# Kernel tuning notes

Measured on AMD Instinct MI355X. Metric: run time of the kernel, lower is better.

Reference implementation:

```python
import jax, jax.numpy as jnp
import numpy as np
import math

ENC_MAX = 64
DEC_MAX = 128


def _tran_mask(M):
    # faithful reconstruction of self.tran and self.mask buffers
    fs = math.log(DEC_MAX / (DEC_MAX + ENC_MAX))  # fixed_shift_p
    fe = math.log(ENC_MAX / (DEC_MAX + ENC_MAX))  # fixed_emit_p
    i = np.arange(M)[:, None]
    j = np.arange(M)[None, :]
    tran = np.where(i + j < M, (M - (i + j) - 1) * fs + fe, 0.0).astype(np.float32)
    # mask_br: -inf where i+j >= M (anti-diagonal i+j==M-1 stays 0)
    mask = np.where(i + j >= M, -np.inf, 0.0).astype(np.float32)
    return jnp.asarray(tran), jnp.asarray(mask)


def _lstm(xs, Wih, Whh, bih, bhh):
    # xs: [L, in]; torch LSTM gate order i,f,g,o; batch=1 handled as unbatched
    H = Whh.shape[1]
    def step(carry, xt):
        h, c = carry
        g = Wih @ xt + bih + Whh @ h + bhh  # [4H]
        i, f, gg, o = jnp.split(g, 4)
        c = jax.nn.sigmoid(f) * c + jax.nn.sigmoid(i) * jnp.tanh(gg)
        h = jax.nn.sigmoid(o) * jnp.tanh(c)
        return (h, c), h
    _, hs = jax.lax.scan(step, (jnp.zeros((H,), xs.dtype), jnp.zeros((H,), xs.dtype)), xs)
    return hs  # [L, H]


def setup_inputs() -> dict:
    key = jax.random.key(0)
    ks = jax.random.split(key, 16)
    V, E, H, K, T = 32000, 100, 512, ENC_MAX, DEC_MAX
    def p(k, shape, scale):
        return jax.random.normal(k, shape, dtype=jnp.float32) * scale
    return {
        "x": jax.random.randint(ks[0], (1, K), 0, V),
        "y": jax.random.randint(ks[1], (1, T), 0, V),
        "emb": p(ks[2], (V, E), 0.1),
        "enc_Wih": p(ks[3], (4 * H, E), 1.0 / np.sqrt(E)),
        "enc_Whh": p(ks[4], (4 * H, H), 1.0 / np.sqrt(H)),
        "enc_bih": jnp.zeros((4 * H,), jnp.float32),
        "enc_bhh": jnp.zeros((4 * H,), jnp.float32),
        "dec_Wih": p(ks[5], (4 * H, E), 1.0 / np.sqrt(E)),
        "dec_Whh": p(ks[6], (4 * H, H), 1.0 / np.sqrt(H)),
        "dec_bih": jnp.zeros((4 * H,), jnp.float32),
        "dec_bhh": jnp.zeros((4 * H,), jnp.float32),
        "Weh": p(ks[7], (E, 2 * H), 1.0 / np.sqrt(2 * H)),  # emit_hidden
        "beh": jnp.zeros((E,), jnp.float32),
        "Wem": p(ks[8], (V, E), 1.0 / np.sqrt(E)),  # emit
        "bem": jnp.zeros((V,), jnp.float32),
    }


def reference(x, y, emb, enc_Wih, enc_Whh, enc_bih, enc_bhh,
              dec_Wih, dec_Whh, dec_bih, dec_bhh, Weh, beh, Wem, bem):
    K = x.shape[1]
    T = y.shape[1]
    x_emb = emb[x[0]]            # [K, E]
    y_emb = emb[y[0]]            # [T, E]
    Eenc = _lstm(x_emb, enc_Wih, enc_Whh, enc_bih, enc_bhh)  # [K, H]
    D = _lstm(y_emb, dec_Wih, dec_Whh, dec_bih, dec_bhh)     # [T, H]

    tran, mask = _tran_mask(ENC_MAX)
    tranm = tran[ENC_MAX - K:, :K] + mask[ENC_MAX - K:, :K]  # [K, K]

    # emissions for all steps at once (joint = cat(E, D_{t-1}) -> relu -> emit -> log_softmax -> gather word_t)
    H = Eenc.shape[1]
    We_E, We_D = Weh[:, :H], Weh[:, H:]
    hpre = jax.nn.relu(Eenc @ We_E.T + (D[:T - 1] @ We_D.T)[:, None, :] + beh)  # [T-1, K, E]
    logits = jnp.einsum('tke,ve->tkv', hpre, Wem) + bem                          # [T-1, K, V]
    words = y[0, 1:]                                                             # [T-1]
    gathered = jnp.take_along_axis(logits, words[:, None, None], axis=2)[..., 0]  # [T-1, K]
    emission = gathered - jax.scipy.special.logsumexp(logits, axis=2)             # [T-1, K]

    def step(pre_alpha, em_t):
        scores = pre_alpha[:, None] + tranm            # [K(i), K(j)]
        mx = jnp.max(scores, axis=0)                   # [K]
        ind = jnp.argmax(scores, axis=0).astype(jnp.int32)
        mx = jnp.flip(mx)                              # self.flip
        ind = jnp.flip(ind)
        new = mx + em_t
        return new, ind

    pre_alpha, inds = jax.lax.scan(step, jnp.zeros((K,), jnp.float32), emission)
    indices = jnp.concatenate([jnp.zeros((1, K), jnp.int32), inds], axis=0)  # [T, K]

    val = pre_alpha[K - 1]  # align_last

    def bstep(ind, idx_row):
        nind = idx_row[ind]
        return nind, nind
    _, alignments = jax.lax.scan(bstep, jnp.int32(K - 1), indices, reverse=True)  # [T]
    return alignments, val
```

## Files before the change

kernel.cpp:

```cpp
#include <hip/hip_runtime.h>


#define K_ENC 64
#define HID   512
#define EMB   100
#define VOC   32000
#define G4    2048

typedef __attribute__((ext_vector_type(8))) short  short8;
typedef __attribute__((ext_vector_type(4))) float  f32x4;
typedef __attribute__((ext_vector_type(4))) int    i32x4;
typedef unsigned long long u64;

#define LOG2E 1.4426950408889634f
#define LN2   0.6931471805599453f

__device__ __forceinline__ unsigned short f2bf(float f) {
  union { float f; unsigned u; } x; x.f = f;
  unsigned r = x.u + 0x7FFFu + ((x.u >> 16) & 1u);
  return (unsigned short)(r >> 16);
}

__device__ __forceinline__ float fast_sigmoid(float x) {
  return __builtin_amdgcn_rcpf(1.f + __builtin_amdgcn_exp2f(-LOG2E * x));
}
__device__ __forceinline__ float fast_tanh(float x) {
  return 1.f - 2.f * __builtin_amdgcn_rcpf(1.f + __builtin_amdgcn_exp2f(2.f * LOG2E * x));
}

#define OFF_PAD   0
#define OFF_HBUF  256
#define OFF_G0E   4352
#define OFF_G0D   135424
#define OFF_EENC  395520
#define OFF_D     428288
#define OFF_EWE   493312
#define OFF_DWD   499712
#define OFF_BEM   512412
#define OFF_SUM   544412
#define OFF_EM    552540
#define OFF_WEM   560668

#define PREP_G0_BLKS 1528
__global__ __launch_bounds__(256) void kPrep0(const int* __restrict__ x, const int* __restrict__ y,
                    const float* __restrict__ emb,
                    const float* __restrict__ eWih, const float* __restrict__ ebih,
                    const float* __restrict__ ebhh,
                    const float* __restrict__ dWih, const float* __restrict__ dbih,
                    const float* __restrict__ dbhh,
                    float* __restrict__ ws) {
  const int b = blockIdx.x;
  const int tid = threadIdx.x;
  if (b < PREP_G0_BLKS) {
    int gid = b * 256 + tid;
    const int enc_total = K_ENC * G4;
    if (gid >= enc_total + 127 * G4) return;
    bool enc = gid < enc_total;
    int loc = enc ? gid : gid - enc_total;
    int t = loc >> 11, r = loc & (G4 - 1);
    int tok = enc ? x[t] : y[t];
    const float* Wr = (enc ? eWih : dWih) + r * EMB;
    const float* er = emb + tok * EMB;
    float s = 0.f;
    #pragma unroll 4
    for (int e = 0; e < EMB; ++e) s += er[e] * Wr[e];
    s += enc ? (ebih[r] + ebhh[r]) : (dbih[r] + dbhh[r]);
    ws[(enc ? OFF_G0E : OFF_G0D) + t * G4 + r] = s;
  } else {
    int gid = (b - PREP_G0_BLKS) * 256 + tid;
    if (gid < 4352) ws[gid] = 0.f;
    else if (gid < 4352 + 127 * 64) ws[OFF_SUM + gid - 4352] = 0.f;
  }
}

#define STEP_GUARD 16384

__global__ __launch_bounds__(512, 2) void kLstm(const float* __restrict__ eWhh,
                                                const float* __restrict__ dWhh,
                                                const float* __restrict__ Wem,
                                                const float* __restrict__ bem,
                                                float* __restrict__ ws) {
  const int b = blockIdx.x;
  const int tid = threadIdx.x;
  if (b >= 64) {
    int gid = (b - 64) * 512 + tid;
    int vt = gid >> 11;
    int kb = (gid >> 9) & 3;
    int L  = (gid >> 3) & 63;
    int j  = gid & 7;
    int v = vt * 16 + (L & 15);
    int k = kb * 32 + ((L >> 4) << 3) + j;
    float val = (k < EMB) ? Wem[v * EMB + k] : 0.f;
    ((unsigned short*)(ws + OFF_WEM))[gid] = f2bf(val);
    if (gid < VOC) ws[OFF_BEM + gid] = bem[gid] * LOG2E;
    return;
  }
  const int grp = b >> 5;
  const int wg  = b & 31;
  const float* __restrict__ Whh = grp ? dWhh : eWhh;
  const float* __restrict__ G0  = ws + (grp ? OFF_G0D : OFF_G0E);
  float* hs = ws + (grp ? OFF_D : OFF_EENC);
  u64* hb = (u64*)(ws + OFF_HBUF) + grp * 1024;
  const int steps = grp ? 127 : K_ENC;
  const int jl = tid >> 5, sub = tid & 31;
  const int j = wg * 16 + jl;
  __shared__ float h_lds[32 * 20];

  float cst = 0.f;
  for (int t = 0; t < steps; ++t) {
    float4 w4[16];
    #pragma unroll
    for (int g = 0; g < 4; ++g)
      #pragma unroll
      for (int q = 0; q < 4; ++q)
        w4[g * 4 + q] = *(const float4*)&Whh[(g * HID + j) * HID + sub * 16 + q * 4];
    float g0i = G0[t * G4 + j];
    float g0f = G0[t * G4 + HID + j];
    float g0g = G0[t * G4 + 2 * HID + j];
    float g0o = G0[t * G4 + 3 * HID + j];
    if (tid < 256) {
      const u64* src = hb + (t & 1) * 512 + tid * 2;
      i32x4 v;
      int guard = 0;
      for (;;) {
        asm volatile("global_load_dwordx4 %0, %1, off sc0 sc1\n\t"
                     "s_waitcnt vmcnt(0)"
                     : "=v"(v) : "v"(src) : "memory");
        if ((v[1] == t && v[3] == t) || ++guard >= STEP_GUARD) break;
        __builtin_amdgcn_s_sleep(1);
      }
      int k0 = tid * 2, k1 = k0 + 1;
      union { int u; float f; } c0, c1; c0.u = v[0]; c1.u = v[2];
      h_lds[(k0 >> 4) * 20 + (k0 & 15)] = c0.f;
      h_lds[(k1 >> 4) * 20 + (k1 & 15)] = c1.f;
    }
    __syncthreads();
    float h[16];
    #pragma unroll
    for (int kk = 0; kk < 16; ++kk) h[kk] = h_lds[sub * 20 + kk];
    float p0 = 0.f, p1 = 0.f, p2 = 0.f, p3 = 0.f;
    #pragma unroll
    for (int q = 0; q < 4; ++q) {
      p0 += w4[0+q].x*h[q*4+0] + w4[0+q].y*h[q*4+1] + w4[0+q].z*h[q*4+2] + w4[0+q].w*h[q*4+3];
      p1 += w4[4+q].x*h[q*4+0] + w4[4+q].y*h[q*4+1] + w4[4+q].z*h[q*4+2] + w4[4+q].w*h[q*4+3];
      p2 += w4[8+q].x*h[q*4+0] + w4[8+q].y*h[q*4+1] + w4[8+q].z*h[q*4+2] + w4[8+q].w*h[q*4+3];
      p3 += w4[12+q].x*h[q*4+0] + w4[12+q].y*h[q*4+1] + w4[12+q].z*h[q*4+2] + w4[12+q].w*h[q*4+3];
    }
    #pragma unroll
    for (int d = 1; d <= 16; d <<= 1) {
      p0 += __shfl_xor(p0, d); p1 += __shfl_xor(p1, d);
      p2 += __shfl_xor(p2, d); p3 += __shfl_xor(p3, d);
    }
    float si = fast_sigmoid(g0i + p0);
    float sf = fast_sigmoid(g0f + p1);
    float gG = fast_tanh(g0g + p2);
    float so = fast_sigmoid(g0o + p3);
    cst = sf * cst + si * gG;
    float hn = so * fast_tanh(cst);
    if (sub == 0) {
      union { float f; unsigned u; } hu; hu.f = hn;
      u64 pack = ((u64)(unsigned)(t + 1) << 32) | (u64)hu.u;
      atomicExch(&hb[((t + 1) & 1) * 512 + j], pack);
      hs[t * HID + j] = hn;
    }
    __syncthreads();
  }
}

__global__ __launch_bounds__(256) void kProj(const float* __restrict__ Weh,
                                             const float* __restrict__ beh,
                                             float* __restrict__ ws) {
  int bid = blockIdx.x;
  bool enc = bid < K_ENC;
  int row = enc ? bid : bid - K_ENC;
  const float* in = ws + (enc ? OFF_EENC : OFF_D) + row * HID;
  __shared__ float sin_[HID];
  int tid = threadIdx.x;
  sin_[tid] = in[tid]; sin_[tid + 256] = in[tid + 256];
  __syncthreads();
  if (tid < EMB) {
    const float* wr = Weh + tid * 1024 + (enc ? 0 : HID);
    float s = 0.f;
    #pragma unroll 4
    for (int h = 0; h < HID; ++h) s += sin_[h] * wr[h];
    if (!enc) s += beh[tid];
    ws[(enc ? OFF_EWE : OFF_DWD) + row * EMB + tid] = s * LOG2E;
  }
}

__global__ __launch_bounds__(256) void kLogits(float* __restrict__ ws) {
  const int tg = blockIdx.x >> 3;
  const int chunk = blockIdx.x & 7;
  const int tid = threadIdx.x;
  const int lane = tid & 63;
  const int wv = tid >> 6;
  const int quad = lane >> 4, l15 = lane & 15;
  __shared__ __align__(16) unsigned short A[2][64 * 128];
  const float* EWe = ws + OFF_EWE;
  const int t0 = tg * 2;
  const int t1v = (t0 + 1 <= 126) ? (t0 + 1) : 126;
  const float* DWd0 = ws + OFF_DWD + t0 * EMB;
  const float* DWd1 = ws + OFF_DWD + t1v * EMB;
  for (int idx = tid; idx < 64 * 128; idx += 256) {
    int m = idx >> 7, k = idx & 127;
    float hv0 = 0.f, hv1 = 0.f;
    if (k < EMB) {
      float e = EWe[m * EMB + k];
      float s0 = e + DWd0[k]; hv0 = s0 > 0.f ? s0 : 0.f;
      float s1 = e + DWd1[k]; hv1 = s1 > 0.f ? s1 : 0.f;
    }
    A[0][idx] = f2bf(hv0);
    A[1][idx] = f2bf(hv1);
  }
  __syncthreads();
  short8 af[2][4][4];
  #pragma unroll
  for (int ts = 0; ts < 2; ++ts)
    #pragma unroll
    for (int mt = 0; mt < 4; ++mt)
      #pragma unroll
      for (int kb = 0; kb < 4; ++kb)
        af[ts][mt][kb] = *(const short8*)&A[ts][(mt * 16 + l15) * 128 + kb * 32 + quad * 8];
  const unsigned short* wem = (const unsigned short*)(ws + OFF_WEM);
  const float* bem_s = ws + OFF_BEM;
  float rs[2][4][4];
  #pragma unroll
  for (int ts = 0; ts < 2; ++ts)
    #pragma unroll
    for (int a = 0; a < 4; ++a)
      #pragma unroll
      for (int c = 0; c < 4; ++c) rs[ts][a][c] = 0.f;
  int vt = chunk * 250 + wv;
  short8 nb0, nb1, nb2, nb3; float nbi;
  nb0 = *(const short8*)&wem[(vt * 4 + 0) * 512 + lane * 8];
  nb1 = *(const short8*)&wem[(vt * 4 + 1) * 512 + lane * 8];
  nb2 = *(const short8*)&wem[(vt * 4 + 2) * 512 + lane * 8];
  nb3 = *(const short8*)&wem[(vt * 4 + 3) * 512 + lane * 8];
  nbi = bem_s[vt * 16 + l15];
  for (int ii = wv; ii < 250; ii += 4) {
    short8 cb0 = nb0, cb1 = nb1, cb2 = nb2, cb3 = nb3;
    float cbi = nbi;
    int nvt = vt + 4;
    if (ii + 4 < 250) {
      nb0 = *(const short8*)&wem[(nvt * 4 + 0) * 512 + lane * 8];
      nb1 = *(const short8*)&wem[(nvt * 4 + 1) * 512 + lane * 8];
      nb2 = *(const short8*)&wem[(nvt * 4 + 2) * 512 + lane * 8];
      nb3 = *(const short8*)&wem[(nvt * 4 + 3) * 512 + lane * 8];
      nbi = bem_s[nvt * 16 + l15];
    }
    #pragma unroll
    for (int ts = 0; ts < 2; ++ts) {
      f32x4 acc[4];
      #pragma unroll
      for (int mt = 0; mt < 4; ++mt) acc[mt] = (f32x4){cbi, cbi, cbi, cbi};
      #pragma unroll
      for (int mt = 0; mt < 4; ++mt) {
        acc[mt] = __builtin_amdgcn_mfma_f32_16x16x32_bf16(af[ts][mt][0], cb0, acc[mt], 0, 0, 0);
        acc[mt] = __builtin_amdgcn_mfma_f32_16x16x32_bf16(af[ts][mt][1], cb1, acc[mt], 0, 0, 0);
        acc[mt] = __builtin_amdgcn_mfma_f32_16x16x32_bf16(af[ts][mt][2], cb2, acc[mt], 0, 0, 0);
        acc[mt] = __builtin_amdgcn_mfma_f32_16x16x32_bf16(af[ts][mt][3], cb3, acc[mt], 0, 0, 0);
      }
      #pragma unroll
      for (int mt = 0; mt < 4; ++mt)
        #pragma unroll
        for (int r = 0; r < 4; ++r)
          rs[ts][mt][r] += __builtin_amdgcn_exp2f(acc[mt][r]);
    }
    vt = nvt;
  }
  #pragma unroll
  for (int d = 1; d < 16; d <<= 1)
    #pragma unroll
    for (int ts = 0; ts < 2; ++ts)
      #pragma unroll
      for (int mt = 0; mt < 4; ++mt)
        #pragma unroll
        for (int r = 0; r < 4; ++r)
          rs[ts][mt][r] += __shfl_xor(rs[ts][mt][r], d);
  if (l15 == 0) {
    #pragma unroll
    for (int ts = 0; ts < 2; ++ts) {
      int t = t0 + ts;
      if (t <= 126) {
        float* sum = ws + OFF_SUM + t * 64;
        #pragma unroll
        for (int mt = 0; mt < 4; ++mt)
          #pragma unroll
          for (int r = 0; r < 4; ++r)
            atomicAdd(&sum[mt * 16 + quad * 4 + r], rs[ts][mt][r]);
      }
    }
  }
}

__global__ __launch_bounds__(256) void kEmission(const int* __restrict__ y,
                                                 const float* __restrict__ Wem,
                                                 float* __restrict__ ws) {
  int gid = blockIdx.x * 256 + threadIdx.x;
  if (gid >= 127 * 64) return;
  int t = gid >> 6, m = gid & 63;
  const float* ew = ws + OFF_EWE + m * EMB;
  const float* dw = ws + OFF_DWD + t * EMB;
  int wt = y[t + 1];
  const float* wr = Wem + wt * EMB;
  float s = ws[OFF_BEM + wt];
  #pragma unroll 4
  for (int e = 0; e < EMB; ++e) {
    float h = ew[e] + dw[e];
    h = h > 0.f ? h : 0.f;
    s += h * wr[e];
  }
  ws[OFF_EM + gid] = LN2 * (s - __builtin_amdgcn_logf(ws[OFF_SUM + gid]));
}

__global__ __launch_bounds__(256) void kViterbi(const float* __restrict__ ws, float* __restrict__ out) {
  __shared__ float em_lds[127 * 64];
  __shared__ int   inds[128 * 64];
  __shared__ float sval;
  const int tid = threadIdx.x;
  for (int i = tid; i < 127 * 64; i += 256) em_lds[i] = ws[OFF_EM + i];
  if (tid < 64) inds[tid] = 0;
  __syncthreads();
  if (tid < 64) {
    const int j = tid;
    const float fs = -0.4054651081081644f;
    const float fe = -1.0986122886681098f;
    float pa = 0.f;
    float emnext = em_lds[j];
    for (int t = 0; t < 127; ++t) {
      float emc = emnext;
      if (t < 126) emnext = em_lds[(t + 1) * 64 + j];
      float v = fmaf(-fs, (float)j, pa);
      int idx = j;
      #pragma unroll
      for (int d = 1; d < 64; d <<= 1) {
        float vv = __shfl_up(v, d);
        int   ii = __shfl_up(idx, d);
        bool cur = v > vv;
        v   = cur ? v : vv;
        idx = cur ? idx : ii;
      }
      pa = v + fe + fs * (float)j + emc;
      inds[(t + 1) * 64 + j] = idx;
    }
    if (j == 63) sval = pa;
  }
  __syncthreads();
  if (tid == 0) {
    int ind = 63;
    for (int t = 127; t >= 0; --t) {
      ind = inds[t * 64 + ind];
      out[t] = (float)ind;
    }
    out[128] = sval;
  }
}

extern "C" void kernel_launch(void* const* d_in, const int* in_sizes, int n_in,
                              void* d_out, int out_size, void* d_ws, size_t ws_size,
                              hipStream_t stream) {
  const int*   x    = (const int*)d_in[0];
  const int*   y    = (const int*)d_in[1];
  const float* emb  = (const float*)d_in[2];
  const float* eWih = (const float*)d_in[3];
  const float* eWhh = (const float*)d_in[4];
  const float* ebih = (const float*)d_in[5];
  const float* ebhh = (const float*)d_in[6];
  const float* dWih = (const float*)d_in[7];
  const float* dWhh = (const float*)d_in[8];
  const float* dbih = (const float*)d_in[9];
  const float* dbhh = (const float*)d_in[10];
  const float* Weh  = (const float*)d_in[11];
  const float* beh  = (const float*)d_in[12];
  const float* Wem  = (const float*)d_in[13];
  const float* bem  = (const float*)d_in[14];
  float* ws  = (float*)d_ws;
  float* out = (float*)d_out;

  hipLaunchKernelGGL(kPrep0,    dim3(PREP_G0_BLKS + 49), dim3(256), 0, stream,
                     x, y, emb, eWih, ebih, ebhh, dWih, dbih, dbhh, ws);
  hipLaunchKernelGGL(kLstm,     dim3(64 + 8000), dim3(512), 0, stream, eWhh, dWhh, Wem, bem, ws);
  hipLaunchKernelGGL(kProj,     dim3(191),   dim3(256), 0, stream, Weh, beh, ws);
  hipLaunchKernelGGL(kLogits,   dim3(512),   dim3(256), 0, stream, ws);
  hipLaunchKernelGGL(kEmission, dim3(32),    dim3(256), 0, stream, y, Wem, ws);
  hipLaunchKernelGGL(kViterbi,  dim3(1),     dim3(256), 0, stream, ws, out);
}
```

Before: 507.8 us.

## Fuse emit-hidden projection into LSTM recurrence and pad logits LDS rows

Removes the separate kProj launch. The projection of each hidden state onto Weh now runs inside the persistent LSTM blocks: the upper four waves of each block compute up to four projection outputs from the h vector already staged in LDS, one step behind, with one extra loop iteration to finish the last row. This saves a kernel launch and re-reading the hidden states, at the cost of one more spin-wait step and extra register pressure in the latency-critical recurrence. Separately, kLogits pads its LDS A-tile rows to 136 elements to reduce bank conflicts on the short8 fragment loads.

```diff
diff --git a/kernel.cpp b/kernel.cpp
--- a/kernel.cpp
+++ b/kernel.cpp
@@ -79,6 +79,8 @@
                                                 const float* __restrict__ dWhh,
                                                 const float* __restrict__ Wem,
                                                 const float* __restrict__ bem,
+                                                const float* __restrict__ Weh,
+                                                const float* __restrict__ beh,
                                                 float* __restrict__ ws) {
   const int b = blockIdx.x;
   const int tid = threadIdx.x;
@@ -100,24 +102,43 @@
   const float* __restrict__ Whh = grp ? dWhh : eWhh;
   const float* __restrict__ G0  = ws + (grp ? OFF_G0D : OFF_G0E);
   float* hs = ws + (grp ? OFF_D : OFF_EENC);
+  float* proj = ws + (grp ? OFF_DWD : OFF_EWE);
   u64* hb = (u64*)(ws + OFF_HBUF) + grp * 1024;
   const int steps = grp ? 127 : K_ENC;
   const int jl = tid >> 5, sub = tid & 31;
   const int j = wg * 16 + jl;
+  const int wv = tid >> 6;
   __shared__ float h_lds[32 * 20];
 
+  const int e = wg * 4 + (wv - 4);
+  const bool do_proj = (wv >= 4) && (e < EMB);
+  float pwf[16];
+  float pbias = 0.f;
+  if (do_proj) {
+    const float* wr = Weh + e * 1024 + (grp ? HID : 0) + sub * 16;
+    #pragma unroll
+    for (int q = 0; q < 4; ++q) {
+      float4 w = *(const float4*)(wr + q * 4);
+      pwf[q*4+0] = w.x; pwf[q*4+1] = w.y; pwf[q*4+2] = w.z; pwf[q*4+3] = w.w;
+    }
+    if (grp) pbias = beh[e];
+  }
+
   float cst = 0.f;
-  for (int t = 0; t < steps; ++t) {
+  for (int t = 0; t <= steps; ++t) {
     float4 w4[16];
-    #pragma unroll
-    for (int g = 0; g < 4; ++g)
-      #pragma unroll
-      for (int q = 0; q < 4; ++q)
-        w4[g * 4 + q] = *(const float4*)&Whh[(g * HID + j) * HID + sub * 16 + q * 4];
-    float g0i = G0[t * G4 + j];
-    float g0f = G0[t * G4 + HID + j];
-    float g0g = G0[t * G4 + 2 * HID + j];
-    float g0o = G0[t * G4 + 3 * HID + j];
+    float g0i = 0.f, g0f = 0.f, g0g = 0.f, g0o = 0.f;
+    if (t < steps) {
+      #pragma unroll
+      for (int g = 0; g < 4; ++g)
+        #pragma unroll
+        for (int q = 0; q < 4; ++q)
+          w4[g * 4 + q] = *(const float4*)&Whh[(g * HID + j) * HID + sub * 16 + q * 4];
+      g0i = G0[t * G4 + j];
+      g0f = G0[t * G4 + HID + j];
+      g0g = G0[t * G4 + 2 * HID + j];
+      g0o = G0[t * G4 + 3 * HID + j];
+    }
     if (tid < 256) {
       const u64* src = hb + (t & 1) * 512 + tid * 2;
       i32x4 v;
@@ -138,56 +159,46 @@
     float h[16];
     #pragma unroll
     for (int kk = 0; kk < 16; ++kk) h[kk] = h_lds[sub * 20 + kk];
-    float p0 = 0.f, p1 = 0.f, p2 = 0.f, p3 = 0.f;
-    #pragma unroll
-    for (int q = 0; q < 4; ++q) {
-      p0 += w4[0+q].x*h[q*4+0] + w4[0+q].y*h[q*4+1] + w4[0+q].z*h[q*4+2] + w4[0+q].w*h[q*4+3];
-      p1 += w4[4+q].x*h[q*4+0] + w4[4+q].y*h[q*4+1] + w4[4+q].z*h[q*4+2] + w4[4+q].w*h[q*4+3];
-      p2 += w4[8+q].x*h[q*4+0] + w4[8+q].y*h[q*4+1] + w4[8+q].z*h[q*4+2] + w4[8+q].w*h[q*4+3];
-      p3 += w4[12+q].x*h[q*4+0] + w4[12+q].y*h[q*4+1] + w4[12+q].z*h[q*4+2] + w4[12+q].w*h[q*4+3];
-    }
-    #pragma unroll
-    for (int d = 1; d <= 16; d <<= 1) {
-      p0 += __shfl_xor(p0, d); p1 += __shfl_xor(p1, d);
-      p2 += __shfl_xor(p2, d); p3 += __shfl_xor(p3, d);
-    }
-    float si = fast_sigmoid(g0i + p0);
-    float sf = fast_sigmoid(g0f + p1);
-    float gG = fast_tanh(g0g + p2);
-    float so = fast_sigmoid(g0o + p3);
-    cst = sf * cst + si * gG;
-    float hn = so * fast_tanh(cst);
-    if (sub == 0) {
-      union { float f; unsigned u; } hu; hu.f = hn;
-      u64 pack = ((u64)(unsigned)(t + 1) << 32) | (u64)hu.u;
-      atomicExch(&hb[((t + 1) & 1) * 512 + j], pack);
-      hs[t * HID + j] = hn;
+    if (t < steps) {
+      float p0 = 0.f, p1 = 0.f, p2 = 0.f, p3 = 0.f;
+      #pragma unroll
+      for (int q = 0; q < 4; ++q) {
+        p0 += w4[0+q].x*h[q*4+0] + w4[0+q].y*h[q*4+1] + w4[0+q].z*h[q*4+2] + w4[0+q].w*h[q*4+3];
+        p1 += w4[4+q].x*h[q*4+0] + w4[4+q].y*h[q*4+1] + w4[4+q].z*h[q*4+2] + w4[4+q].w*h[q*4+3];
+        p2 += w4[8+q].x*h[q*4+0] + w4[8+q].y*h[q*4+1] + w4[8+q].z*h[q*4+2] + w4[8+q].w*h[q*4+3];
+        p3 += w4[12+q].x*h[q*4+0] + w4[12+q].y*h[q*4+1] + w4[12+q].z*h[q*4+2] + w4[12+q].w*h[q*4+3];
+      }
+      #pragma unroll
+      for (int d = 1; d <= 16; d <<= 1) {
+        p0 += __shfl_xor(p0, d); p1 += __shfl_xor(p1, d);
+        p2 += __shfl_xor(p2, d); p3 += __shfl_xor(p3, d);
+      }
+      float si = fast_sigmoid(g0i + p0);
+      float sf = fast_sigmoid(g0f + p1);
+      float gG = fast_tanh(g0g + p2);
+      float so = fast_sigmoid(g0o + p3);
+      cst = sf * cst + si * gG;
+      float hn = so * fast_tanh(cst);
+      if (sub == 0) {
+        union { float f; unsigned u; } hu; hu.f = hn;
+        u64 pack = ((u64)(unsigned)(t + 1) << 32) | (u64)hu.u;
+        atomicExch(&hb[((t + 1) & 1) * 512 + j], pack);
+        hs[t * HID + j] = hn;
+      }
+    }
+    if (t >= 1 && do_proj) {
+      float p = 0.f;
+      #pragma unroll
+      for (int kk = 0; kk < 16; ++kk) p += h[kk] * pwf[kk];
+      #pragma unroll
+      for (int d = 1; d <= 16; d <<= 1) p += __shfl_xor(p, d);
+      if ((tid & 63) == 0) proj[(t - 1) * EMB + e] = (p + pbias) * LOG2E;
     }
     __syncthreads();
   }
 }
 
-__global__ __launch_bounds__(256) void kProj(const float* __restrict__ Weh,
-                                             const float* __restrict__ beh,
-                                             float* __restrict__ ws) {
-  int bid = blockIdx.x;
-  bool enc = bid < K_ENC;
-  int row = enc ? bid : bid - K_ENC;
-  const float* in = ws + (enc ? OFF_EENC : OFF_D) + row * HID;
-  __shared__ float sin_[HID];
-  int tid = threadIdx.x;
-  sin_[tid] = in[tid]; sin_[tid + 256] = in[tid + 256];
-  __syncthreads();
-  if (tid < EMB) {
-    const float* wr = Weh + tid * 1024 + (enc ? 0 : HID);
-    float s = 0.f;
-    #pragma unroll 4
-    for (int h = 0; h < HID; ++h) s += sin_[h] * wr[h];
-    if (!enc) s += beh[tid];
-    ws[(enc ? OFF_EWE : OFF_DWD) + row * EMB + tid] = s * LOG2E;
-  }
-}
-
+#define AP 136
 __global__ __launch_bounds__(256) void kLogits(float* __restrict__ ws) {
   const int tg = blockIdx.x >> 3;
   const int chunk = blockIdx.x & 7;
@@ -195,7 +206,7 @@
   const int lane = tid & 63;
   const int wv = tid >> 6;
   const int quad = lane >> 4, l15 = lane & 15;
-  __shared__ __align__(16) unsigned short A[2][64 * 128];
+  __shared__ __align__(16) unsigned short A[2][64 * AP];
   const float* EWe = ws + OFF_EWE;
   const int t0 = tg * 2;
   const int t1v = (t0 + 1 <= 126) ? (t0 + 1) : 126;
@@ -209,8 +220,8 @@
       float s0 = e + DWd0[k]; hv0 = s0 > 0.f ? s0 : 0.f;
       float s1 = e + DWd1[k]; hv1 = s1 > 0.f ? s1 : 0.f;
     }
-    A[0][idx] = f2bf(hv0);
-    A[1][idx] = f2bf(hv1);
+    A[0][m * AP + k] = f2bf(hv0);
+    A[1][m * AP + k] = f2bf(hv1);
   }
   __syncthreads();
   short8 af[2][4][4];
@@ -220,7 +231,7 @@
     for (int mt = 0; mt < 4; ++mt)
       #pragma unroll
       for (int kb = 0; kb < 4; ++kb)
-        af[ts][mt][kb] = *(const short8*)&A[ts][(mt * 16 + l15) * 128 + kb * 32 + quad * 8];
+        af[ts][mt][kb] = *(const short8*)&A[ts][(mt * 16 + l15) * AP + kb * 32 + quad * 8];
   const unsigned short* wem = (const unsigned short*)(ws + OFF_WEM);
   const float* bem_s = ws + OFF_BEM;
   float rs[2][4][4];
@@ -379,8 +390,8 @@
 
   hipLaunchKernelGGL(kPrep0,    dim3(PREP_G0_BLKS + 49), dim3(256), 0, stream,
                      x, y, emb, eWih, ebih, ebhh, dWih, dbih, dbhh, ws);
-  hipLaunchKernelGGL(kLstm,     dim3(64 + 8000), dim3(512), 0, stream, eWhh, dWhh, Wem, bem, ws);
-  hipLaunchKernelGGL(kProj,     dim3(191),   dim3(256), 0, stream, Weh, beh, ws);
+  hipLaunchKernelGGL(kLstm,     dim3(64 + 8000), dim3(512), 0, stream,
+                     eWhh, dWhh, Wem, bem, Weh, beh, ws);
   hipLaunchKernelGGL(kLogits,   dim3(512),   dim3(256), 0, stream, ws);
   hipLaunchKernelGGL(kEmission, dim3(32),    dim3(256), 0, stream, y, Wem, ws);
   hipLaunchKernelGGL(kViterbi,  dim3(1),     dim3(256), 0, stream, ws, out);
```

New measurement: 686.0 us. 1.35x slower.
